# Performance work log

Hardware: AMD Instinct MI355X
Metric: run time of the kernel (lower is better)

The kernel has to match this reference:

```python
import jax, jax.numpy as jnp
import numpy as np

N_NODES = 8192
N_EDGES = 100000
N_PAIRS = 1000000
PATH_LEN = 8
EDGE_DIM = 16


def setup_inputs() -> dict:
    key = jax.random.key(0)
    k1, k2, k3, k4, k5 = jax.random.split(key, 5)
    edge_attr = jax.random.normal(k1, (N_EDGES, EDGE_DIM), dtype=jnp.float32)
    src = jax.random.randint(k2, (N_PAIRS,), 0, N_NODES)
    dst = jax.random.randint(k3, (N_PAIRS,), 0, N_NODES)
    # -1 denotes path padding, as in the torch module's mask = (path != -1)
    paths = jax.random.randint(k4, (N_PAIRS, PATH_LEN), -1, N_EDGES)
    edge_vector = jax.random.normal(k5, (PATH_LEN, EDGE_DIM), dtype=jnp.float32)
    return {"num_nodes": N_NODES, "edge_attr": edge_attr, "src": src,
            "dst": dst, "paths": paths, "edge_vector": edge_vector}


def reference(num_nodes, edge_attr, src, dst, paths, edge_vector):
    # paths: (P, L) with -1 padding; edge_attr: (E, D); edge_vector: (L, D)
    mask = (paths != -1).astype(edge_attr.dtype)          # (P, L)
    idx = jnp.clip(paths, 0)                              # (P, L)
    ef = edge_attr[idx]                                   # (P, L, D) gather
    dots = jnp.einsum('pld,ld->pl', ef, edge_vector) * mask  # (P, L)
    dots = dots.mean(axis=1)                              # mean over full path length (matches torch)
    cij = jnp.zeros((num_nodes, num_nodes), dtype=edge_attr.dtype)
    cij = cij.at[src, dst].set(dots)                      # indexed assignment scatter
    return cij
```

## Files before the change

kernel.cpp:

```cpp
#include <hip/hip_runtime.h>
#include <hip/hip_fp16.h>
#include <math.h>


#define NN   8192
#define ROW4 (NN / 4)
#define CAP  256

typedef float nfloat4 __attribute__((ext_vector_type(4)));

__global__ void k_edot(const float4* __restrict__ ea, const float4* __restrict__ ev,
                       __half* __restrict__ D, unsigned* __restrict__ cnt, int E) {
    __shared__ float4 sev[32];
    if (threadIdx.x < 32) sev[threadIdx.x] = ev[threadIdx.x];
    __syncthreads();
    int e = blockIdx.x * blockDim.x + threadIdx.x;
    if (e < NN) cnt[e] = 0u;
    if (e >= E) return;
    const float4* row = ea + (size_t)e * 4;
    float4 a0 = row[0], a1 = row[1], a2 = row[2], a3 = row[3];
    float out[8];
#pragma unroll
    for (int l = 0; l < 8; ++l) {
        float4 v0 = sev[l * 4 + 0], v1 = sev[l * 4 + 1];
        float4 v2 = sev[l * 4 + 2], v3 = sev[l * 4 + 3];
        float acc = a0.x * v0.x + a0.y * v0.y + a0.z * v0.z + a0.w * v0.w;
        acc += a1.x * v1.x + a1.y * v1.y + a1.z * v1.z + a1.w * v1.w;
        acc += a2.x * v2.x + a2.y * v2.y + a2.z * v2.z + a2.w * v2.w;
        acc += a3.x * v3.x + a3.y * v3.y + a3.z * v3.z + a3.w * v3.w;
        out[l] = acc;
    }
    union { unsigned u[4]; uint4 v; } pk;
#pragma unroll
    for (int q = 0; q < 4; ++q) {
        __half2 h2 = __floats2half2_rn(out[2 * q], out[2 * q + 1]);
        pk.u[q] = *(unsigned*)&h2;
    }
    ((uint4*)D)[e] = pk.v;
}

__global__ void k_dots_bin(const __half* __restrict__ D, const int4* __restrict__ paths,
                           const int4* __restrict__ src4, const int4* __restrict__ dst4,
                           unsigned* __restrict__ cnt,
                           unsigned long long* __restrict__ recs, int P) {
    int g = blockIdx.x * blockDim.x + threadIdx.x;
    int p0 = g * 4;
    if (p0 >= P) return;
    int4 sv = src4[g];
    int4 dv = dst4[g];
    int ss[4] = {sv.x, sv.y, sv.z, sv.w};
    int dd[4] = {dv.x, dv.y, dv.z, dv.w};

#pragma unroll
    for (int q = 0; q < 4; ++q) {
        int p = p0 + q;
        if (p >= P) break;
        int4 i0 = paths[(size_t)p * 2 + 0];
        int4 i1 = paths[(size_t)p * 2 + 1];
        int idxs[8] = {i0.x, i0.y, i0.z, i0.w, i1.x, i1.y, i1.z, i1.w};
        float acc = 0.0f;
#pragma unroll
        for (int l = 0; l < 8; ++l) {
            int idx = idxs[l];
            if (idx >= 0)
                acc += __half2float(D[(size_t)idx * 8 + l]);
        }
        acc *= 0.125f;

        unsigned r = (unsigned)ss[q];
        unsigned pos = atomicAdd(&cnt[r], 1u);
        if (pos < CAP) {
            unsigned long long rec =
                ((unsigned long long)(unsigned)dd[q] << 51) |
                ((unsigned long long)(unsigned)(p + 1) << 31) |
                (unsigned long long)(__float_as_uint(acc) >> 1);
            recs[(size_t)r * CAP + pos] = rec;
        }
    }
}

__global__ __launch_bounds__(256) void k_emit(const unsigned long long* __restrict__ recs,
                                              const unsigned* __restrict__ cnt,
                                              float* __restrict__ out) {
    __shared__ unsigned img[NN];
    int r = blockIdx.x, t = threadIdx.x;
    uint4* img4 = (uint4*)img;
#pragma unroll
    for (int i = t; i < ROW4; i += 256) img4[i] = make_uint4(0u, 0u, 0u, 0u);
    __syncthreads();

    unsigned c = cnt[r]; if (c > CAP) c = CAP;
    unsigned long long rec = 0; unsigned d = 0, key = 0;
    bool has = (unsigned)t < c;
    if (has) {
        rec = recs[(size_t)r * CAP + t];
        d   = (unsigned)(rec >> 51);
        key = (unsigned)((rec >> 31) & 0xFFFFFu);
        atomicMax(&img[d], key);
    }
    __syncthreads();
    bool win = has && (img[d] == key);
    __syncthreads();
    if (win) img[d] = (unsigned)(rec & 0x7FFFFFFFull);
    __syncthreads();

    size_t base = (size_t)r * ROW4;
    nfloat4* out4 = (nfloat4*)out;
#pragma unroll
    for (int i = t; i < ROW4; i += 256) {
        uint4 v = img4[i];
        nfloat4 o;
        o.x = __uint_as_float(v.x << 1);
        o.y = __uint_as_float(v.y << 1);
        o.z = __uint_as_float(v.z << 1);
        o.w = __uint_as_float(v.w << 1);
        __builtin_nontemporal_store(o, &out4[base + i]);
    }
}

extern "C" void kernel_launch(void* const* d_in, const int* in_sizes, int n_in,
                              void* d_out, int out_size, void* d_ws, size_t ws_size,
                              hipStream_t stream) {
    const float* edge_attr = (const float*)d_in[1];
    const int*   src       = (const int*)d_in[2];
    const int*   dst       = (const int*)d_in[3];
    const int*   paths     = (const int*)d_in[4];
    const float* ev        = (const float*)d_in[5];
    int P = in_sizes[2];
    int E = in_sizes[1] / 16;

    char* w = (char*)d_ws;
    size_t o1 = ((size_t)NN * 4 + 255) & ~255ull;
    size_t o2 = (o1 + (size_t)E * 8 * 2 + 255) & ~255ull;
    unsigned*           cnt  = (unsigned*)w;
    __half*             D    = (__half*)(w + o1);
    unsigned long long* recs = (unsigned long long*)(w + o2);

    const int B = 256;
    k_edot<<<(E + B - 1) / B, B, 0, stream>>>((const float4*)edge_attr,
                                              (const float4*)ev, D, cnt, E);
    int G4 = (P / 4 + B - 1) / B;
    k_dots_bin<<<G4, B, 0, stream>>>(D, (const int4*)paths, (const int4*)src,
                                     (const int4*)dst, cnt, recs, P);
    k_emit<<<NN, B, 0, stream>>>(recs, cnt, (float*)d_out);
}
```

Baseline: 382.0 us.

## Fuse edge-dot, binning and emit into one cooperative persistent kernel

Replaces the three separate kernel launches with one cooperative kernel of 1024 blocks that runs the edge-dot, pair binning and row-emit phases in sequence, separated by grid-wide syncs. The per-row emit becomes a grid-stride loop over rows that reuses the block's shared-memory image. The aim is to remove the launch gaps and tail effects between the stages. In exchange it adds grid-sync cost, limits the emit phase to 4 resident blocks per CU, and switches the binning loads from vectorized 4-pair loads to scalar loads. The old three-kernel path is kept as a fallback if the cooperative launch fails.

```diff
diff --git a/kernel.cpp b/kernel.cpp
--- a/kernel.cpp
+++ b/kernel.cpp
@@ -1,13 +1,126 @@
 #include <hip/hip_runtime.h>
 #include <hip/hip_fp16.h>
+#include <hip/hip_cooperative_groups.h>
 #include <math.h>
+
+namespace cg = cooperative_groups;
 
 
 #define NN   8192
 #define ROW4 (NN / 4)
 #define CAP  256
+#define GRID 1024
+#define TPB  256
+#define NTHREADS (GRID * TPB)
 
 typedef float nfloat4 __attribute__((ext_vector_type(4)));
+
+__global__ __launch_bounds__(TPB, 4) void k_fused(
+    const float4* __restrict__ ea, const float4* __restrict__ ev,
+    __half* __restrict__ D, unsigned* __restrict__ cnt,
+    unsigned long long* __restrict__ recs,
+    const int* __restrict__ src, const int* __restrict__ dst,
+    const int4* __restrict__ paths, float* __restrict__ out,
+    int E, int P)
+{
+    __shared__ unsigned img[NN];
+    cg::grid_group grid = cg::this_grid();
+    int t = threadIdx.x;
+    int g = blockIdx.x * TPB + t;
+
+    {
+        float4* sev = (float4*)img;
+        if (t < 32) sev[t] = ev[t];
+        __syncthreads();
+        if (g < NN) cnt[g] = 0u;
+        if (g < E) {
+            const float4* row = ea + (size_t)g * 4;
+            float4 a0 = row[0], a1 = row[1], a2 = row[2], a3 = row[3];
+            float o[8];
+#pragma unroll
+            for (int l = 0; l < 8; ++l) {
+                float4 v0 = sev[l * 4 + 0], v1 = sev[l * 4 + 1];
+                float4 v2 = sev[l * 4 + 2], v3 = sev[l * 4 + 3];
+                float acc = a0.x * v0.x + a0.y * v0.y + a0.z * v0.z + a0.w * v0.w;
+                acc += a1.x * v1.x + a1.y * v1.y + a1.z * v1.z + a1.w * v1.w;
+                acc += a2.x * v2.x + a2.y * v2.y + a2.z * v2.z + a2.w * v2.w;
+                acc += a3.x * v3.x + a3.y * v3.y + a3.z * v3.z + a3.w * v3.w;
+                o[l] = acc;
+            }
+            union { unsigned u[4]; uint4 v; } pk;
+#pragma unroll
+            for (int q = 0; q < 4; ++q) {
+                __half2 h2 = __floats2half2_rn(o[2 * q], o[2 * q + 1]);
+                pk.u[q] = *(unsigned*)&h2;
+            }
+            ((uint4*)D)[g] = pk.v;
+        }
+    }
+    __threadfence();
+    grid.sync();
+
+    for (int p = g; p < P; p += NTHREADS) {
+        int4 i0 = paths[(size_t)p * 2 + 0];
+        int4 i1 = paths[(size_t)p * 2 + 1];
+        int idxs[8] = {i0.x, i0.y, i0.z, i0.w, i1.x, i1.y, i1.z, i1.w};
+        float acc = 0.0f;
+#pragma unroll
+        for (int l = 0; l < 8; ++l) {
+            int idx = idxs[l];
+            if (idx >= 0)
+                acc += __half2float(D[(size_t)idx * 8 + l]);
+        }
+        acc *= 0.125f;
+
+        unsigned r = (unsigned)src[p];
+        unsigned pos = atomicAdd(&cnt[r], 1u);
+        if (pos < CAP) {
+            unsigned long long rec =
+                ((unsigned long long)(unsigned)dst[p] << 51) |
+                ((unsigned long long)(unsigned)(p + 1) << 31) |
+                (unsigned long long)(__float_as_uint(acc) >> 1);
+            recs[(size_t)r * CAP + pos] = rec;
+        }
+    }
+    __threadfence();
+    grid.sync();
+
+    uint4* img4 = (uint4*)img;
+    for (int r = blockIdx.x; r < NN; r += GRID) {
+#pragma unroll
+        for (int i = t; i < ROW4; i += TPB) img4[i] = make_uint4(0u, 0u, 0u, 0u);
+        __syncthreads();
+
+        unsigned c = cnt[r]; if (c > CAP) c = CAP;
+        unsigned long long rec = 0; unsigned d = 0, key = 0;
+        bool has = (unsigned)t < c;
+        if (has) {
+            rec = recs[(size_t)r * CAP + t];
+            d   = (unsigned)(rec >> 51);
+            key = (unsigned)((rec >> 31) & 0xFFFFFu);
+            atomicMax(&img[d], key);
+        }
+        __syncthreads();
+        bool win = has && (img[d] == key);
+        __syncthreads();
+        if (win) img[d] = (unsigned)(rec & 0x7FFFFFFFull);
+        __syncthreads();
+
+        size_t base = (size_t)r * ROW4;
+        nfloat4* out4 = (nfloat4*)out;
+#pragma unroll
+        for (int i = t; i < ROW4; i += TPB) {
+            uint4 v = img4[i];
+            nfloat4 o;
+            o.x = __uint_as_float(v.x << 1);
+            o.y = __uint_as_float(v.y << 1);
+            o.z = __uint_as_float(v.z << 1);
+            o.w = __uint_as_float(v.w << 1);
+            __builtin_nontemporal_store(o, &out4[base + i]);
+        }
+        __syncthreads();
+    }
+}
 
 __global__ void k_edot(const float4* __restrict__ ea, const float4* __restrict__ ev,
                        __half* __restrict__ D, unsigned* __restrict__ cnt, int E) {
@@ -19,21 +132,20 @@
     if (e >= E) return;
     const float4* row = ea + (size_t)e * 4;
     float4 a0 = row[0], a1 = row[1], a2 = row[2], a3 = row[3];
-    float out[8];
+    float o[8];
 #pragma unroll
     for (int l = 0; l < 8; ++l) {
-        float4 v0 = sev[l * 4 + 0], v1 = sev[l * 4 + 1];
-        float4 v2 = sev[l * 4 + 2], v3 = sev[l * 4 + 3];
-        float acc = a0.x * v0.x + a0.y * v0.y + a0.z * v0.z + a0.w * v0.w;
-        acc += a1.x * v1.x + a1.y * v1.y + a1.z * v1.z + a1.w * v1.w;
-        acc += a2.x * v2.x + a2.y * v2.y + a2.z * v2.z + a2.w * v2.w;
-        acc += a3.x * v3.x + a3.y * v3.y + a3.z * v3.z + a3.w * v3.w;
-        out[l] = acc;
+        float4 v0 = sev[l*4+0], v1 = sev[l*4+1], v2 = sev[l*4+2], v3 = sev[l*4+3];
+        float acc = a0.x*v0.x + a0.y*v0.y + a0.z*v0.z + a0.w*v0.w;
+        acc += a1.x*v1.x + a1.y*v1.y + a1.z*v1.z + a1.w*v1.w;
+        acc += a2.x*v2.x + a2.y*v2.y + a2.z*v2.z + a2.w*v2.w;
+        acc += a3.x*v3.x + a3.y*v3.y + a3.z*v3.z + a3.w*v3.w;
+        o[l] = acc;
     }
     union { unsigned u[4]; uint4 v; } pk;
 #pragma unroll
     for (int q = 0; q < 4; ++q) {
-        __half2 h2 = __floats2half2_rn(out[2 * q], out[2 * q + 1]);
+        __half2 h2 = __floats2half2_rn(o[2*q], o[2*q+1]);
         pk.u[q] = *(unsigned*)&h2;
     }
     ((uint4*)D)[e] = pk.v;
@@ -50,7 +162,6 @@
     int4 dv = dst4[g];
     int ss[4] = {sv.x, sv.y, sv.z, sv.w};
     int dd[4] = {dv.x, dv.y, dv.z, dv.w};
-
 #pragma unroll
     for (int q = 0; q < 4; ++q) {
         int p = p0 + q;
@@ -62,11 +173,9 @@
 #pragma unroll
         for (int l = 0; l < 8; ++l) {
             int idx = idxs[l];
-            if (idx >= 0)
-                acc += __half2float(D[(size_t)idx * 8 + l]);
+            if (idx >= 0) acc += __half2float(D[(size_t)idx * 8 + l]);
         }
         acc *= 0.125f;
-
         unsigned r = (unsigned)ss[q];
         unsigned pos = atomicAdd(&cnt[r], 1u);
         if (pos < CAP) {
@@ -88,7 +197,6 @@
 #pragma unroll
     for (int i = t; i < ROW4; i += 256) img4[i] = make_uint4(0u, 0u, 0u, 0u);
     __syncthreads();
-
     unsigned c = cnt[r]; if (c > CAP) c = CAP;
     unsigned long long rec = 0; unsigned d = 0, key = 0;
     bool has = (unsigned)t < c;
@@ -103,7 +211,6 @@
     __syncthreads();
     if (win) img[d] = (unsigned)(rec & 0x7FFFFFFFull);
     __syncthreads();
-
     size_t base = (size_t)r * ROW4;
     nfloat4* out4 = (nfloat4*)out;
 #pragma unroll
@@ -136,11 +243,23 @@
     __half*             D    = (__half*)(w + o1);
     unsigned long long* recs = (unsigned long long*)(w + o2);
 
-    const int B = 256;
-    k_edot<<<(E + B - 1) / B, B, 0, stream>>>((const float4*)edge_attr,
-                                              (const float4*)ev, D, cnt, E);
-    int G4 = (P / 4 + B - 1) / B;
-    k_dots_bin<<<G4, B, 0, stream>>>(D, (const int4*)paths, (const int4*)src,
-                                     (const int4*)dst, cnt, recs, P);
-    k_emit<<<NN, B, 0, stream>>>(recs, cnt, (float*)d_out);
-}
+    const float4* ea4 = (const float4*)edge_attr;
+    const float4* ev4 = (const float4*)ev;
+    const int4*   pt4 = (const int4*)paths;
+    float*        outp = (float*)d_out;
+
+    void* args[] = {(void*)&ea4, (void*)&ev4, (void*)&D, (void*)&cnt,
+                    (void*)&recs, (void*)&src, (void*)&dst, (void*)&pt4,
+                    (void*)&outp, (void*)&E, (void*)&P};
+    hipError_t err = hipLaunchCooperativeKernel((const void*)k_fused,
+                                                dim3(GRID), dim3(TPB),
+                                                args, 0, stream);
+    if (err != hipSuccess) {
+        const int B = 256;
+        k_edot<<<(E + B - 1) / B, B, 0, stream>>>(ea4, ev4, D, cnt, E);
+        int G4 = (P / 4 + B - 1) / B;
+        k_dots_bin<<<G4, B, 0, stream>>>(D, pt4, (const int4*)src,
+                                         (const int4*)dst, cnt, recs, P);
+        k_emit<<<NN, B, 0, stream>>>(recs, cnt, outp);
+    }
+}
```

New measurement: 767.9 us. +101.0%, slower.
